# Optimization experiments

Hardware: AMD Instinct MI355X
Metric: run time of the kernel (lower is better)

## Reference

```python
import jax, jax.numpy as jnp
import numpy as np

HEADS = 4
DIM_HEAD = 64
SCALE = 10.0
EPS = 1e-12  # matches torch F.normalize default eps


def setup_inputs() -> dict:
    key = jax.random.key(0)
    k1, k2, k3, k4, k5 = jax.random.split(key, 5)
    dim = 256
    hidden = HEADS * DIM_HEAD
    x = jax.random.normal(k1, (16, dim, 32, 32), dtype=jnp.float32)
    y = jax.random.normal(k2, (16, dim, 32, 32), dtype=jnp.float32)
    # 1x1 conv weights stored as 2D matrices (out_ch, in_ch)
    w_qkv = jax.random.normal(k3, (hidden * 3, dim), dtype=jnp.float32) * (1.0 / np.sqrt(dim))
    w_out = jax.random.normal(k4, (dim, hidden), dtype=jnp.float32) * (1.0 / np.sqrt(hidden))
    b_out = jax.random.normal(k5, (dim,), dtype=jnp.float32) * 0.01
    return {"x": x, "y": y, "w_qkv": w_qkv, "w_out": w_out, "b_out": b_out}


def _l2norm(t):
    # torch F.normalize(t, dim=-1): t / max(||t||_2, eps)
    n = jnp.sqrt(jnp.sum(t * t, axis=-1, keepdims=True))
    return t / jnp.maximum(n, EPS)


def reference(x, y, w_qkv, w_out, b_out):
    b, c, hh, ww = x.shape
    n_x = hh * ww
    n_y = y.shape[2] * y.shape[3]
    hidden = HEADS * DIM_HEAD

    # 1x1 convs == channel matmuls; only q from x and k,v from y are used
    w_q, w_k, w_v = w_qkv[:hidden], w_qkv[hidden:2 * hidden], w_qkv[2 * hidden:]
    q = jnp.einsum('oc,bcn->bon', w_q, x.reshape(b, c, n_x)).reshape(b, HEADS, DIM_HEAD, n_x)
    k = jnp.einsum('oc,bcn->bon', w_k, y.reshape(b, c, n_y)).reshape(b, HEADS, DIM_HEAD, n_y)
    v = jnp.einsum('oc,bcn->bon', w_v, y.reshape(b, c, n_y)).reshape(b, HEADS, DIM_HEAD, n_y)

    # l2norm over the spatial (last) axis, as in the source
    q = _l2norm(q)
    k = _l2norm(k)

    sim = jnp.einsum('bhdi,bhdj->bhij', q, k) * SCALE          # [b,h,n_x,n_y]
    attn = jax.nn.softmax(sim, axis=-1)
    out = jnp.einsum('bhij,bhdj->bhid', attn, v)                # [b,h,n_x,d]

    # 'b h (x y) d -> b (h d) x y'
    out = out.transpose(0, 1, 3, 2).reshape(b, hidden, hh, ww)
    out = jnp.einsum('oc,bcn->bon', w_out, out.reshape(b, hidden, n_x))
    out = out + b_out[None, :, None]
    return out.reshape(b, -1, hh, ww)
```

## Files before the change

### kernel.cpp

```cpp
#include <hip/hip_runtime.h>
#include <hip/hip_bf16.h>
#include <stdint.h>

typedef __attribute__((ext_vector_type(8))) short short8;
typedef __attribute__((ext_vector_type(4))) float f32x4;
typedef __attribute__((ext_vector_type(4))) unsigned short ushort4v;

#define MFMA16(a, b, c) __builtin_amdgcn_mfma_f32_16x16x32_bf16((a), (b), (c), 0, 0, 0)


__device__ __forceinline__ ushort f2bf(float f) {
  union { float f; unsigned u; } x; x.f = f;
  unsigned r = x.u + 0x7FFFu + ((x.u >> 16) & 1u);
  return (ushort)(r >> 16);
}

__device__ __forceinline__ short8 ld8(const ushort* p) {
  return *reinterpret_cast<const short8*>(p);
}

__device__ __forceinline__ void gll16(const void* g, void* l) {
  __builtin_amdgcn_global_load_lds(
      reinterpret_cast<const __attribute__((address_space(1))) unsigned int*>(
          reinterpret_cast<uintptr_t>(g)),
      reinterpret_cast<__attribute__((address_space(3))) unsigned int*>(
          reinterpret_cast<uintptr_t>(l)),
      16, 0, 0);
}

__device__ __forceinline__ void stage_tile(const char* gbase, char* ldsbase,
                                           int goff, int ldsw) {
#pragma unroll
  for (int c = 0; c < 8; ++c)
    gll16(gbase + c * 8192 + goff, ldsbase + c * 8192 + ldsw);
}

__global__ __launch_bounds__(256) void k_tcvt(const float* __restrict__ x,
    const float* __restrict__ y, ushort* __restrict__ xbt, ushort* __restrict__ ybt,
    const float* __restrict__ wqkv, const float* __restrict__ wout,
    ushort* __restrict__ wqkvb, ushort* __restrict__ woutb) {
  int tile = blockIdx.x;
  if (tile >= 2048) {
    const int t1 = 49152;
    const int tot = t1 + 16384;
    for (int i = (tile - 2048) * 256 + threadIdx.x; i < tot; i += 64 * 256) {
      if (i < t1) {
        float4 v = reinterpret_cast<const float4*>(wqkv)[i];
        ushort4v u = {f2bf(v.x), f2bf(v.y), f2bf(v.z), f2bf(v.w)};
        reinterpret_cast<ushort4v*>(wqkvb)[i] = u;
      } else {
        int j = i - t1;
        float4 v = reinterpret_cast<const float4*>(wout)[j];
        ushort4v u = {f2bf(v.x), f2bf(v.y), f2bf(v.z), f2bf(v.w)};
        reinterpret_cast<ushort4v*>(woutb)[j] = u;
      }
    }
    return;
  }
  const float* src; ushort* dst;
  if (tile >= 1024) { tile -= 1024; src = y; dst = ybt; }
  else { src = x; dst = xbt; }
  int b = tile >> 6;
  int c0 = ((tile >> 4) & 3) << 6;
  int n0 = (tile & 15) << 6;
  __shared__ ushort ldsT[64][72];
  int tid = threadIdx.x;
  const float* sb = src + ((size_t)b << 18);
  int cc = tid >> 4, n4 = tid & 15;
#pragma unroll
  for (int s = 0; s < 4; ++s) {
    int c = cc + s * 16;
    float4 v = *reinterpret_cast<const float4*>(sb + (size_t)(c0 + c) * 1024 + n0 + n4 * 4);
    ldsT[n4 * 4 + 0][c] = f2bf(v.x);
    ldsT[n4 * 4 + 1][c] = f2bf(v.y);
    ldsT[n4 * 4 + 2][c] = f2bf(v.z);
    ldsT[n4 * 4 + 3][c] = f2bf(v.w);
  }
  __syncthreads();
  ushort* db = dst + ((size_t)b << 18);
  int nn = tid >> 4, c4 = tid & 15;
#pragma unroll
  for (int s = 0; s < 4; ++s) {
    int n = nn + s * 16;
    ushort4v u = *reinterpret_cast<const ushort4v*>(&ldsT[n][c4 * 4]);
    *reinterpret_cast<ushort4v*>(db + (size_t)(n0 + n) * 256 + c0 + c4 * 4) = u;
  }
}

__global__ __launch_bounds__(512, 2) void k_qkv(const ushort* __restrict__ wqkvb,
    const ushort* __restrict__ xbt, const ushort* __restrict__ ybt,
    ushort* __restrict__ qt, ushort* __restrict__ kt, ushort* __restrict__ vbuf) {
  int bid = blockIdx.x;
  int lid = (bid & 7) * 48 + (bid >> 3);
  int ox = lid % 24;
  int b = lid / 24;
  int o0 = ox * 32;
  const ushort* Bsrc = (o0 < 256) ? xbt : ybt;
  const char* Bm = (const char*)(Bsrc + ((size_t)b << 18));
  int tid = threadIdx.x;
  int l = tid & 63, w = tid >> 6;
  int r = l & 15, g = l >> 4;

  __shared__ __align__(16) char Bt[2][65536];
  __shared__ float snorm[8][32];
  __shared__ float fs[32];

  const ushort* Ab = wqkvb + (size_t)(o0 + r) * 256 + g * 8;
  short8 areg[2][8];
#pragma unroll
  for (int ks = 0; ks < 8; ++ks) {
    areg[0][ks] = ld8(Ab + ks * 32);
    areg[1][ks] = ld8(Ab + 4096 + ks * 32);
  }

  int Lb = tid * 16;
  int trow = Lb >> 9;
  int goff = trow * 512 + ((Lb & 511) ^ ((trow & 7) << 4));
  int ldsw = w * 1024;

  f32x4 acc[2][8];
#pragma unroll
  for (int i = 0; i < 2; ++i)
#pragma unroll
    for (int j = 0; j < 8; ++j) acc[i][j] = (f32x4){0.f, 0.f, 0.f, 0.f};

  stage_tile(Bm, &Bt[0][0], goff, ldsw);

  int rr = w * 16 + r;
  int sw = (r & 7) << 4;
  for (int nt = 0; nt < 8; ++nt) {
    int cur = nt & 1;
    if (nt < 7) {
      stage_tile(Bm + (size_t)(nt + 1) * 65536, &Bt[cur ^ 1][0], goff, ldsw);
      asm volatile("s_waitcnt vmcnt(8)" ::: "memory");
    } else {
      asm volatile("s_waitcnt vmcnt(0)" ::: "memory");
    }
    __builtin_amdgcn_sched_barrier(0);
    __builtin_amdgcn_s_barrier();
    const char* Bc = &Bt[cur][0];
#pragma unroll
    for (int ks = 0; ks < 8; ++ks) {
      short8 bv = *reinterpret_cast<const short8*>(Bc + rr * 512 + ((ks * 64 + g * 16) ^ sw));
      acc[0][nt] = MFMA16(areg[0][ks], bv, acc[0][nt]);
      acc[1][nt] = MFMA16(areg[1][ks], bv, acc[1][nt]);
    }
    asm volatile("s_waitcnt lgkmcnt(0)" ::: "memory");
    __builtin_amdgcn_sched_barrier(0);
    __builtin_amdgcn_s_barrier();
  }

  if (o0 < 512) {
    float ss[2][4];
#pragma unroll
    for (int mf = 0; mf < 2; ++mf)
#pragma unroll
      for (int reg = 0; reg < 4; ++reg) {
        float s = 0.f;
#pragma unroll
        for (int nt = 0; nt < 8; ++nt) { float v = acc[mf][nt][reg]; s += v * v; }
#pragma unroll
        for (int m = 1; m < 16; m <<= 1) s += __shfl_xor(s, m);
        ss[mf][reg] = s;
      }
    if (r == 0) {
#pragma unroll
      for (int mf = 0; mf < 2; ++mf)
#pragma unroll
        for (int reg = 0; reg < 4; ++reg)
          snorm[w][mf * 16 + g * 4 + reg] = ss[mf][reg];
    }
    __syncthreads();
    if (tid < 32) {
      float s = 0.f;
#pragma unroll
      for (int w2 = 0; w2 < 8; ++w2) s += snorm[w2][tid];
      fs[tid] = ((o0 < 256) ? 10.0f : 1.0f) / fmaxf(sqrtf(s), 1e-12f);
    }
    __syncthreads();
    float fr[2][4];
#pragma unroll
    for (int mf = 0; mf < 2; ++mf)
#pragma unroll
      for (int reg = 0; reg < 4; ++reg) fr[mf][reg] = fs[mf * 16 + g * 4 + reg];
    int od = (o0 < 256) ? o0 : o0 - 256;
    int hh = od >> 6, d0 = od & 63;
    ushort* dst = ((o0 < 256) ? qt : kt) + (((size_t)(b * 4 + hh)) << 16);
#pragma unroll
    for (int mf = 0; mf < 2; ++mf)
#pragma unroll
      for (int nt = 0; nt < 8; ++nt) {
        int n = nt * 128 + w * 16 + r;
        ushort4v u;
#pragma unroll
        for (int reg = 0; reg < 4; ++reg) u[reg] = f2bf(acc[mf][nt][reg] * fr[mf][reg]);
        *reinterpret_cast<ushort4v*>(dst + (size_t)n * 64 + d0 + mf * 16 + g * 4) = u;
      }
  } else {
#pragma unroll
    for (int mf = 0; mf < 2; ++mf) {
      int ob = o0 - 512 + mf * 16 + g * 4;
#pragma unroll
      for (int nt = 0; nt < 8; ++nt) {
        int n = nt * 128 + w * 16 + r;
#pragma unroll
        for (int reg = 0; reg < 4; ++reg)
          vbuf[(((size_t)b * 256 + ob + reg) << 10) + n] = f2bf(acc[mf][nt][reg]);
      }
    }
  }
}

__global__ __launch_bounds__(512, 4) void k_attn(const ushort* __restrict__ qt,
    const ushort* __restrict__ kt, const ushort* __restrict__ vbuf,
    ushort* __restrict__ aot) {
  int hb = blockIdx.x;
  int it = blockIdx.y;
  int h = hb & 3, b = hb >> 2;
  int tid = threadIdx.x;
  int l = tid & 63, w = tid >> 6;
  int r = l & 15, g = l >> 4;
  size_t ho = ((size_t)hb) << 16;
  const ushort* Q = qt + ho;
  const char* Kg = (const char*)(kt + ho);
  const char* Vg = (const char*)(vbuf + ((size_t)b << 18) + ((size_t)h << 16));
  int i0 = it * 128 + w * 16;

  __shared__ __align__(16) ushort Kb[3][4096];
  __shared__ __align__(16) ushort Vb[3][4096];
  __shared__ __align__(16) ushort plds[8][1024];

  int L = w * 1024 + l * 16;
  int srow = L >> 7;
  int swz = (srow & 7) << 4;
  int ksrc = L ^ swz;
  int vsrc_col = (L & 127) ^ swz;

  short8 qa[2];
#pragma unroll
  for (int ks = 0; ks < 2; ++ks)
    qa[ks] = ld8(Q + (size_t)(i0 + r) * 64 + ks * 32 + g * 8);

  f32x4 oacc[4];
  float rsum[4];
#pragma unroll
  for (int j = 0; j < 4; ++j) { oacc[j] = (f32x4){0.f, 0.f, 0.f, 0.f}; rsum[j] = 0.f; }

#define STAGE(buf, j0v) do { \
    gll16(Kg + (j0v) * 128 + ksrc, (char*)&Kb[buf][0] + w * 1024); \
    gll16(Vg + (size_t)srow * 2048 + (j0v) * 2 + vsrc_col, (char*)&Vb[buf][0] + w * 1024); \
  } while (0)

  STAGE(0, 0);
  STAGE(1, 64);

  char* plc = (char*)plds[w];
  int cur = 0;
  for (int t = 0; t < 16; ++t) {
    if (t < 15) asm volatile("s_waitcnt vmcnt(2)" ::: "memory");
    else        asm volatile("s_waitcnt vmcnt(0)" ::: "memory");
    __builtin_amdgcn_sched_barrier(0);
    asm volatile("s_barrier" ::: "memory");
    __builtin_amdgcn_sched_barrier(0);
    if (t < 14) {
      int nb3 = cur + 2; if (nb3 >= 3) nb3 -= 3;
      STAGE(nb3, (t + 2) * 64);
    }
    const char* Kc = (const char*)&Kb[cur][0];
    const char* Vc = (const char*)&Vb[cur][0];
    f32x4 sacc[4];
#pragma unroll
    for (int nf = 0; nf < 4; ++nf) sacc[nf] = (f32x4){0.f, 0.f, 0.f, 0.f};
    __builtin_amdgcn_s_setprio(1);
#pragma unroll
    for (int nf = 0; nf < 4; ++nf) {
      int row = nf * 16 + r;
      int sw = (row & 7) << 4;
      short8 k0 = *reinterpret_cast<const short8*>(Kc + ((row * 128 + g * 16) ^ sw));
      short8 k1 = *reinterpret_cast<const short8*>(Kc + ((row * 128 + 64 + g * 16) ^ sw));
      sacc[nf] = MFMA16(qa[0], k0, sacc[nf]);
      sacc[nf] = MFMA16(qa[1], k1, sacc[nf]);
    }
    __builtin_amdgcn_s_setprio(0);
#pragma unroll
    for (int nf = 0; nf < 4; ++nf)
#pragma unroll
      for (int reg = 0; reg < 4; ++reg) {
        float p = __expf(sacc[nf][reg]);
        rsum[reg] += p;
        union { float f; unsigned u; } cv; cv.f = p;
        int row = g * 4 + reg;
        int xorv = ((row ^ (row >> 3)) & 7) << 4;
        int byteo = row * 128 + (((nf * 16 + r) * 2) ^ xorv);
        *(ushort*)(plc + byteo) = (ushort)(cv.u >> 16);
      }
    short8 pa[2];
#pragma unroll
    for (int ks = 0; ks < 2; ++ks) {
      int xorv = (r ^ (r >> 3)) & 7;
      int blk = (ks * 4 + g) ^ xorv;
      pa[ks] = *reinterpret_cast<const short8*>(plc + r * 128 + blk * 16);
    }
    __builtin_amdgcn_s_setprio(1);
#pragma unroll
    for (int df = 0; df < 4; ++df) {
      int row = df * 16 + r;
      int sw = (row & 7) << 4;
#pragma unroll
      for (int ks = 0; ks < 2; ++ks) {
        short8 vf = *reinterpret_cast<const short8*>(Vc + ((row * 128 + ks * 64 + g * 16) ^ sw));
        oacc[df] = MFMA16(pa[ks], vf, oacc[df]);
      }
    }
    __builtin_amdgcn_s_setprio(0);
    cur += 1; if (cur >= 3) cur -= 3;
  }
#undef STAGE

#pragma unroll
  for (int reg = 0; reg < 4; ++reg) {
    float s = rsum[reg];
#pragma unroll
    for (int m = 1; m < 16; m <<= 1) s += __shfl_xor(s, m);
    rsum[reg] = 1.0f / s;
  }
#pragma unroll
  for (int df = 0; df < 4; ++df)
#pragma unroll
    for (int reg = 0; reg < 4; ++reg) {
      int i = i0 + g * 4 + reg;
      int d = df * 16 + r;
      float vo = oacc[df][reg] * rsum[reg];
      aot[((size_t)b << 18) + (size_t)i * 256 + h * 64 + d] = f2bf(vo);
    }
}

__global__ __launch_bounds__(512, 2) void k_out(const ushort* __restrict__ woutb,
    const ushort* __restrict__ aot, const float* __restrict__ bout,
    float* __restrict__ out) {
  int bid = blockIdx.x;
  int lid = (bid & 7) * 32 + (bid >> 3);
  int ox = lid & 7;
  int t2 = lid >> 3;
  int nb = t2 & 1;
  int b = t2 >> 1;
  int o0 = ox * 32;
  int tid = threadIdx.x, l = tid & 63, w = tid >> 6, r = l & 15, g = l >> 4;
  const char* Bm = (const char*)(aot + ((size_t)b << 18) + ((size_t)nb << 17));

  __shared__ __align__(16) char Bt[2][65536];

  const ushort* Ab = woutb + (size_t)(o0 + r) * 256 + g * 8;
  short8 areg[2][8];
#pragma unroll
  for (int ks = 0; ks < 8; ++ks) {
    areg[0][ks] = ld8(Ab + ks * 32);
    areg[1][ks] = ld8(Ab + 4096 + ks * 32);
  }

  int Lb = tid * 16;
  int trow = Lb >> 9;
  int goff = trow * 512 + ((Lb & 511) ^ ((trow & 7) << 4));
  int ldsw = w * 1024;

  f32x4 acc[2][4];
#pragma unroll
  for (int i = 0; i < 2; ++i)
#pragma unroll
    for (int j = 0; j < 4; ++j) acc[i][j] = (f32x4){0.f, 0.f, 0.f, 0.f};

  stage_tile(Bm, &Bt[0][0], goff, ldsw);

  int rr = w * 16 + r;
  int sw = (r & 7) << 4;
  for (int nt = 0; nt < 4; ++nt) {
    int cur = nt & 1;
    if (nt < 3) {
      stage_tile(Bm + (size_t)(nt + 1) * 65536, &Bt[cur ^ 1][0], goff, ldsw);
      asm volatile("s_waitcnt vmcnt(8)" ::: "memory");
    } else {
      asm volatile("s_waitcnt vmcnt(0)" ::: "memory");
    }
    __builtin_amdgcn_sched_barrier(0);
    __builtin_amdgcn_s_barrier();
    const char* Bc = &Bt[cur][0];
#pragma unroll
    for (int ks = 0; ks < 8; ++ks) {
      short8 bv = *reinterpret_cast<const short8*>(Bc + rr * 512 + ((ks * 64 + g * 16) ^ sw));
      acc[0][nt] = MFMA16(areg[0][ks], bv, acc[0][nt]);
      acc[1][nt] = MFMA16(areg[1][ks], bv, acc[1][nt]);
    }
    asm volatile("s_waitcnt lgkmcnt(0)" ::: "memory");
    __builtin_amdgcn_sched_barrier(0);
    __builtin_amdgcn_s_barrier();
  }

  float bias[2][4];
#pragma unroll
  for (int mf = 0; mf < 2; ++mf)
#pragma unroll
    for (int reg = 0; reg < 4; ++reg) bias[mf][reg] = bout[o0 + mf * 16 + g * 4 + reg];
#pragma unroll
  for (int mf = 0; mf < 2; ++mf)
#pragma unroll
    for (int nt = 0; nt < 4; ++nt)
#pragma unroll
      for (int reg = 0; reg < 4; ++reg) {
        size_t o = (size_t)(b * 256 + o0 + mf * 16 + g * 4 + reg);
        int n = nb * 512 + nt * 128 + w * 16 + r;
        out[(o << 10) + n] = acc[mf][nt][reg] + bias[mf][reg];
      }
}

extern "C" void kernel_launch(void* const* d_in, const int* in_sizes, int n_in,
                              void* d_out, int out_size, void* d_ws, size_t ws_size,
                              hipStream_t stream) {
  const float* x     = (const float*)d_in[0];
  const float* y     = (const float*)d_in[1];
  const float* wqkv  = (const float*)d_in[2];
  const float* wout  = (const float*)d_in[3];
  const float* bout  = (const float*)d_in[4];
  float* out = (float*)d_out;
  char* ws = (char*)d_ws;

  ushort* xbt   = (ushort*)(ws + 0ull);
  ushort* aot   = (ushort*)(ws + 0ull);
  ushort* ybt   = (ushort*)(ws + 8388608ull);
  ushort* qt    = (ushort*)(ws + 16777216ull);
  ushort* kt    = (ushort*)(ws + 25165824ull);
  ushort* vbuf  = (ushort*)(ws + 33554432ull);
  ushort* wqkvb = (ushort*)(ws + 41943040ull);
  ushort* woutb = (ushort*)(ws + 42336256ull);

  k_tcvt<<<2112, 256, 0, stream>>>(x, y, xbt, ybt, wqkv, wout, wqkvb, woutb);
  k_qkv<<<384, 512, 0, stream>>>(wqkvb, xbt, ybt, qt, kt, vbuf);
  k_attn<<<dim3(64, 8), 512, 0, stream>>>(qt, kt, vbuf, aot);
  k_out<<<256, 512, 0, stream>>>(woutb, aot, bout, out);
}
```

Before: 151.9 us.

## Halve QKV LDS tiles, raise occupancy, and use single-barrier double buffering

The QKV projection kernel now stages half-K tiles (32KB per buffer instead of 64KB), which raises the occupancy hint from 2 to 4 blocks per SU. To cut register pressure it loads the weight A fragments from global memory inside the loop instead of keeping them resident. Both GEMM kernels move the next-tile prefetch to after a single barrier per iteration, dropping the trailing barrier and lgkmcnt wait. The cost is twice as many pipeline iterations, repeated global/L1 weight loads, and a full vmcnt(0) wait before each tile, which shrinks load/compute overlap.

```diff
diff --git a/kernel.cpp b/kernel.cpp
--- a/kernel.cpp
+++ b/kernel.cpp
@@ -33,6 +33,13 @@
 #pragma unroll
   for (int c = 0; c < 8; ++c)
     gll16(gbase + c * 8192 + goff, ldsbase + c * 8192 + ldsw);
+}
+
+__device__ __forceinline__ void stage_tile32(const char* gbase, char* ldsbase,
+                                             int goff, int ldsw) {
+#pragma unroll
+  for (int c = 0; c < 4; ++c)
+    gll16(gbase + c * 16384 + goff, ldsbase + c * 8192 + ldsw);
 }
 
 __global__ __launch_bounds__(256) void k_tcvt(const float* __restrict__ x,
@@ -87,7 +94,7 @@
   }
 }
 
-__global__ __launch_bounds__(512, 2) void k_qkv(const ushort* __restrict__ wqkvb,
+__global__ __launch_bounds__(512, 4) void k_qkv(const ushort* __restrict__ wqkvb,
     const ushort* __restrict__ xbt, const ushort* __restrict__ ybt,
     ushort* __restrict__ qt, ushort* __restrict__ kt, ushort* __restrict__ vbuf) {
   int bid = blockIdx.x;
@@ -101,21 +108,15 @@
   int l = tid & 63, w = tid >> 6;
   int r = l & 15, g = l >> 4;
 
-  __shared__ __align__(16) char Bt[2][65536];
+  __shared__ __align__(16) char Bt[2][32768];
   __shared__ float snorm[8][32];
   __shared__ float fs[32];
 
   const ushort* Ab = wqkvb + (size_t)(o0 + r) * 256 + g * 8;
-  short8 areg[2][8];
-#pragma unroll
-  for (int ks = 0; ks < 8; ++ks) {
-    areg[0][ks] = ld8(Ab + ks * 32);
-    areg[1][ks] = ld8(Ab + 4096 + ks * 32);
-  }
 
   int Lb = tid * 16;
-  int trow = Lb >> 9;
-  int goff = trow * 512 + ((Lb & 511) ^ ((trow & 7) << 4));
+  int trow = Lb >> 8;
+  int goff = trow * 512 + ((Lb & 255) ^ ((trow & 7) << 4));
   int ldsw = w * 1024;
 
   f32x4 acc[2][8];
@@ -124,30 +125,32 @@
 #pragma unroll
     for (int j = 0; j < 8; ++j) acc[i][j] = (f32x4){0.f, 0.f, 0.f, 0.f};
 
-  stage_tile(Bm, &Bt[0][0], goff, ldsw);
+  stage_tile32(Bm, &Bt[0][0], goff, ldsw);
 
   int rr = w * 16 + r;
   int sw = (r & 7) << 4;
-  for (int nt = 0; nt < 8; ++nt) {
-    int cur = nt & 1;
-    if (nt < 7) {
-      stage_tile(Bm + (size_t)(nt + 1) * 65536, &Bt[cur ^ 1][0], goff, ldsw);
-      asm volatile("s_waitcnt vmcnt(8)" ::: "memory");
-    } else {
-      asm volatile("s_waitcnt vmcnt(0)" ::: "memory");
-    }
+  for (int t = 0; t < 16; ++t) {
+    int cur = t & 1;
+    asm volatile("s_waitcnt vmcnt(0)" ::: "memory");
     __builtin_amdgcn_sched_barrier(0);
     __builtin_amdgcn_s_barrier();
+    __builtin_amdgcn_sched_barrier(0);
+    if (t < 15) {
+      int t1 = t + 1;
+      stage_tile32(Bm + (size_t)(t1 >> 1) * 65536 + (t1 & 1) * 256,
+                   &Bt[cur ^ 1][0], goff, ldsw);
+    }
     const char* Bc = &Bt[cur][0];
-#pragma unroll
-    for (int ks = 0; ks < 8; ++ks) {
-      short8 bv = *reinterpret_cast<const short8*>(Bc + rr * 512 + ((ks * 64 + g * 16) ^ sw));
-      acc[0][nt] = MFMA16(areg[0][ks], bv, acc[0][nt]);
-      acc[1][nt] = MFMA16(areg[1][ks], bv, acc[1][nt]);
-    }
-    asm volatile("s_waitcnt lgkmcnt(0)" ::: "memory");
-    __builtin_amdgcn_sched_barrier(0);
-    __builtin_amdgcn_s_barrier();
+    int nchunk = t >> 1, chalf = t & 1;
+#pragma unroll
+    for (int ks4 = 0; ks4 < 4; ++ks4) {
+      int ks = chalf * 4 + ks4;
+      short8 a0 = ld8(Ab + ks * 32);
+      short8 a1 = ld8(Ab + 4096 + ks * 32);
+      short8 bv = *reinterpret_cast<const short8*>(Bc + rr * 256 + ((ks4 * 64 + g * 16) ^ sw));
+      acc[0][nchunk] = MFMA16(a0, bv, acc[0][nchunk]);
+      acc[1][nchunk] = MFMA16(a1, bv, acc[1][nchunk]);
+    }
   }
 
   if (o0 < 512) {
@@ -375,14 +378,11 @@
   int sw = (r & 7) << 4;
   for (int nt = 0; nt < 4; ++nt) {
     int cur = nt & 1;
-    if (nt < 3) {
-      stage_tile(Bm + (size_t)(nt + 1) * 65536, &Bt[cur ^ 1][0], goff, ldsw);
-      asm volatile("s_waitcnt vmcnt(8)" ::: "memory");
-    } else {
-      asm volatile("s_waitcnt vmcnt(0)" ::: "memory");
-    }
+    asm volatile("s_waitcnt vmcnt(0)" ::: "memory");
     __builtin_amdgcn_sched_barrier(0);
     __builtin_amdgcn_s_barrier();
+    __builtin_amdgcn_sched_barrier(0);
+    if (nt < 3) stage_tile(Bm + (size_t)(nt + 1) * 65536, &Bt[cur ^ 1][0], goff, ldsw);
     const char* Bc = &Bt[cur][0];
 #pragma unroll
     for (int ks = 0; ks < 8; ++ks) {
@@ -390,9 +390,6 @@
       acc[0][nt] = MFMA16(areg[0][ks], bv, acc[0][nt]);
       acc[1][nt] = MFMA16(areg[1][ks], bv, acc[1][nt]);
     }
-    asm volatile("s_waitcnt lgkmcnt(0)" ::: "memory");
-    __builtin_amdgcn_sched_barrier(0);
-    __builtin_amdgcn_s_barrier();
   }
 
   float bias[2][4];
```

Measured after the change: 178.6 us. 1.18x slower.
